# Performance work log

Measured on AMD Instinct MI355X. Metric: run time of the kernel, lower is better.

## Reference

```python
import jax, jax.numpy as jnp
import numpy as np

R = 14        # num_relations
N = 100000    # num nodes
E = 1600000   # num edges
B = 8         # n_bases: num_blocks for layer 1, num_bases for layer 2
DIN, DH, DOUT = 64, 64, 64


def setup_inputs() -> dict:
    key = jax.random.key(0)
    ks = jax.random.split(key, 10)
    x = jax.random.normal(ks[0], (N, DIN), jnp.float32)
    edge_index = jax.random.randint(ks[1], (2, E), 0, N)
    edge_type = jax.random.randint(ks[2], (E,), 0, R)
    # Layer 1: block-diagonal decomposition weights (R, B, DIN/B, DH/B)
    w1 = jax.random.normal(ks[3], (R, B, DIN // B, DH // B), jnp.float32) * 0.1
    root1 = jax.random.normal(ks[4], (DIN, DH), jnp.float32) * 0.1
    bias1 = jnp.zeros((DH,), jnp.float32)
    # Layer 2: basis decomposition: W_r = sum_b comp2[r,b] * bases2[b]
    comp2 = jax.random.normal(ks[5], (R, B), jnp.float32) * 0.3
    bases2 = jax.random.normal(ks[6], (B, DH, DOUT), jnp.float32) * 0.1
    root2 = jax.random.normal(ks[7], (DH, DOUT), jnp.float32) * 0.1
    bias2 = jnp.zeros((DOUT,), jnp.float32)
    return {"x": x, "edge_index": edge_index, "edge_type": edge_type,
            "w1": w1, "root1": root1, "bias1": bias1,
            "comp2": comp2, "bases2": bases2, "root2": root2, "bias2": bias2}


def _rel_scatter_max(h_rel, src, dst, edge_type):
    """h_rel: (R, N, d) per-relation transformed node features.
    Per-relation scatter-max over destination nodes, then sum over relations
    (PyG RGCNConv with aggr='max': empty segments contribute 0)."""
    msgs = h_rel[edge_type, src]                  # (E, d) gather
    seg = edge_type * N + dst                     # combined (relation, dst) key
    agg = jax.ops.segment_max(msgs, seg, num_segments=R * N)  # (R*N, d), -inf where empty
    agg = jnp.where(jnp.isneginf(agg), 0.0, agg)
    return agg.reshape(R, N, -1).sum(axis=0)      # (N, d)


def reference(x, edge_index, edge_type, w1, root1, bias1, comp2, bases2, root2, bias2):
    src, dst = edge_index[0], edge_index[1]
    # ---- layer 1: block-diagonal RGCNConv, aggr='max' ----
    xb = x.reshape(N, B, DIN // B)
    h = jnp.einsum('nbi,rbio->rnbo', xb, w1).reshape(R, N, DH)
    out = _rel_scatter_max(h, src, dst, edge_type) + x @ root1 + bias1
    x1 = jax.nn.relu(out)  # dropout p=0.4 is identity in eval mode
    # ---- layer 2: basis-decomposed RGCNConv, aggr='max' ----
    W2 = jnp.einsum('rb,bio->rio', comp2, bases2)  # (R, DH, DOUT)
    h2 = jnp.einsum('ni,rio->rno', x1, W2)         # (R, N, DOUT)
    out2 = _rel_scatter_max(h2, src, dst, edge_type) + x1 @ root2 + bias2
    return out2
```

## Files before the change

kernel.cpp:

```cpp
#include <hip/hip_runtime.h>
#include <math.h>

#define RNUM 14
#define NNODE 100000
#define ENUM 1600000
#define NBKT 196
#define NFINE 8192
#define NBLK1 ((ENUM + 8191) / 8192)
#define NT16 (NNODE / 16)
#define NTB ((NT16 + 15) / 16)

typedef __attribute__((ext_vector_type(8))) short bf16x8;
typedef __attribute__((ext_vector_type(4))) float f32x4;

__device__ inline unsigned short f2bf(float f) {
    unsigned u = __builtin_bit_cast(unsigned, f);
    u += 0x7FFF + ((u >> 16) & 1);
    return (unsigned short)(u >> 16);
}
__device__ inline float bf2f(unsigned short h) {
    unsigned u = ((unsigned)h) << 16;
    return __builtin_bit_cast(float, u);
}
__device__ inline int uload(const int* __restrict__ p) {
    return __builtin_amdgcn_readfirstlane(*p);
}

__global__ void __launch_bounds__(1024) bhist_k(const int* __restrict__ dst,
                                                int* __restrict__ bcnt) {
    __shared__ int c[256];
    int t = threadIdx.x;
    if (t < 256) c[t] = 0;
    __syncthreads();
    int e0 = blockIdx.x * 8192;
#pragma unroll
    for (int j = 0; j < 8; j++) {
        int e = e0 + j * 1024 + t;
        if (e < ENUM) atomicAdd(&c[dst[e] >> 9], 1);
    }
    __syncthreads();
    if (t < NBKT && c[t] > 0) atomicAdd(&bcnt[t], c[t]);
}

__global__ void bscan_k(const int* __restrict__ bcnt, int* __restrict__ bbase,
                        int* __restrict__ bcursor) {
    __shared__ int sh[256];
    int t = threadIdx.x;
    int v = (t < NBKT) ? bcnt[t] : 0;
    sh[t] = v;
    __syncthreads();
    for (int o = 1; o < 256; o <<= 1) {
        int u = (t >= o) ? sh[t - o] : 0;
        __syncthreads();
        sh[t] += u;
        __syncthreads();
    }
    int excl = sh[t] - v;
    if (t < NBKT) { bbase[t] = excl; bcursor[t] = excl; }
    if (t == NBKT - 1) bbase[NBKT] = sh[t];
}

__global__ void __launch_bounds__(1024) scatter1_k(const int* __restrict__ src,
        const int* __restrict__ dst, const int* __restrict__ et,
        int* __restrict__ bcursor, int2* __restrict__ pay) {
    __shared__ int cnt[256];
    __shared__ int rnk[256];
    __shared__ int base[256];
    int t = threadIdx.x;
    if (t < 256) { cnt[t] = 0; rnk[t] = 0; }
    __syncthreads();
    int e0 = blockIdx.x * 8192;
    int d[8], s[8], r[8];
#pragma unroll
    for (int j = 0; j < 8; j++) {
        int e = e0 + j * 1024 + t;
        if (e < ENUM) {
            d[j] = dst[e]; s[j] = src[e]; r[j] = et[e];
            atomicAdd(&cnt[d[j] >> 9], 1);
        } else d[j] = -1;
    }
    __syncthreads();
    if (t < NBKT && cnt[t] > 0) base[t] = atomicAdd(&bcursor[t], cnt[t]);
    __syncthreads();
#pragma unroll
    for (int j = 0; j < 8; j++) {
        if (d[j] < 0) continue;
        int b = d[j] >> 9;
        int rk = atomicAdd(&rnk[b], 1);
        int2 p; p.x = r[j] * NNODE + s[j]; p.y = (d[j] & 511) * 16 + r[j];
        pay[base[b] + rk] = p;
    }
}

__global__ void __launch_bounds__(1024) bsort_k(const int2* __restrict__ pay,
        const int* __restrict__ bbase, int* __restrict__ offs, int* __restrict__ ssrc) {
    __shared__ int cnt[NFINE];
    __shared__ int tsum[1024];
    int bkt = blockIdx.x, t = threadIdx.x;
    int e0 = bbase[bkt], e1 = bbase[bkt + 1];
#pragma unroll
    for (int i = t; i < NFINE; i += 1024) cnt[i] = 0;
    __syncthreads();
    for (int e = e0 + t; e < e1; e += 1024) atomicAdd(&cnt[pay[e].y], 1);
    __syncthreads();
    int loc[8], s = 0;
#pragma unroll
    for (int j = 0; j < 8; j++) { loc[j] = cnt[t * 8 + j]; s += loc[j]; }
    tsum[t] = s;
    __syncthreads();
    for (int o = 1; o < 1024; o <<= 1) {
        int u = (t >= o) ? tsum[t - o] : 0;
        __syncthreads();
        tsum[t] += u;
        __syncthreads();
    }
    int run = tsum[t] - s;
#pragma unroll
    for (int j = 0; j < 8; j++) {
        int idx = t * 8 + j;
        cnt[idx] = run;
        offs[bkt * NFINE + idx] = e0 + run;
        run += loc[j];
    }
    __syncthreads();
    for (int e = e0 + t; e < e1; e += 1024) {
        int2 p = pay[e];
        int rk = atomicAdd(&cnt[p.y], 1);
        ssrc[e0 + rk] = p.x;
    }
}

__global__ void frags_k(const float* __restrict__ w1, const float* __restrict__ comp2,
                        const float* __restrict__ bases2, const float* __restrict__ root1,
                        const float* __restrict__ root2,
                        unsigned short* __restrict__ frag1, unsigned short* __restrict__ frag2,
                        unsigned short* __restrict__ rootf1, unsigned short* __restrict__ rootf2) {
    int gid = blockIdx.x * 256 + threadIdx.x;
    if (gid < 2 * RNUM * 4096) {
        int which = gid >= RNUM * 4096;
        int idx = gid - which * (RNUM * 4096);
        int j = idx & 7, lane = (idx >> 3) & 63, ot = (idx >> 9) & 3, kh = (idx >> 11) & 1, r = idx >> 12;
        int k = kh * 32 + (lane >> 4) * 8 + j;
        int c = ot * 16 + (lane & 15);
        if (!which) {
            int bi = k >> 3, bo = c >> 3;
            float v = 0.f;
            if (bi == bo) v = w1[((r * 8 + bi) * 8 + (k & 7)) * 8 + (c & 7)];
            frag1[idx] = f2bf(v);
        } else {
            float s = 0.f;
#pragma unroll
            for (int b = 0; b < 8; b++) s += comp2[r * 8 + b] * bases2[(b * 64 + k) * 64 + c];
            frag2[idx] = f2bf(s);
        }
    } else {
        int idx2 = gid - 2 * RNUM * 4096;
        if (idx2 >= 8192) return;
        int which = idx2 >= 4096;
        int idx = idx2 & 4095;
        int j = idx & 7, lane = (idx >> 3) & 63, ot = (idx >> 9) & 3, kh = (idx >> 11) & 1;
        int k = kh * 32 + (lane >> 4) * 8 + j;
        int c = ot * 16 + (lane & 15);
        const float* W = which ? root2 : root1;
        unsigned short* F = which ? rootf2 : rootf1;
        F[idx] = f2bf(W[k * 64 + c]);
    }
}

__global__ void xb_k(const float* __restrict__ x, unsigned short* __restrict__ xb) {
    int idx = blockIdx.x * 256 + threadIdx.x;
    if (idx >= NNODE * 64) return;
    xb[idx] = f2bf(x[idx]);
}

__global__ void __launch_bounds__(256) gemm_k(const unsigned short* __restrict__ A,
                                              const unsigned short* __restrict__ F,
                                              unsigned short* __restrict__ Y) {
    int tb = blockIdx.x % NTB;
    int r  = blockIdx.x / NTB;
    int wave = threadIdx.x >> 6, lane = threadIdx.x & 63;
    const unsigned short* Fr = F + (size_t)r * 4096;
    bf16x8 wf[2][4];
#pragma unroll
    for (int kh = 0; kh < 2; kh++)
#pragma unroll
        for (int ot = 0; ot < 4; ot++)
            wf[kh][ot] = *(const bf16x8*)(Fr + ((kh * 4 + ot) * 64 + lane) * 8);
    int node16 = lane & 15;
    int kcol = (lane >> 4) * 8;
    int g = lane >> 4;
    for (int s = 0; s < 4; s++) {
        int nt = tb * 16 + wave * 4 + s;
        if (nt >= NT16) break;
        int nbase = nt * 16;
        const unsigned short* Arow = A + (size_t)(nbase + node16) * 64;
        bf16x8 b0 = *(const bf16x8*)(Arow + kcol);
        bf16x8 b1 = *(const bf16x8*)(Arow + 32 + kcol);
        f32x4 acc[4];
#pragma unroll
        for (int ot = 0; ot < 4; ot++) {
            acc[ot] = (f32x4){0.f, 0.f, 0.f, 0.f};
            acc[ot] = __builtin_amdgcn_mfma_f32_16x16x32_bf16(wf[0][ot], b0, acc[ot], 0, 0, 0);
            acc[ot] = __builtin_amdgcn_mfma_f32_16x16x32_bf16(wf[1][ot], b1, acc[ot], 0, 0, 0);
        }
        unsigned short* Yr = Y + ((size_t)r * NNODE + nbase) * 64;
#pragma unroll
        for (int ot = 0; ot < 4; ot++) {
            unsigned p0 = (unsigned)f2bf(acc[ot][0]) | ((unsigned)f2bf(acc[ot][1]) << 16);
            unsigned p1 = (unsigned)f2bf(acc[ot][2]) | ((unsigned)f2bf(acc[ot][3]) << 16);
            uint2 pv; pv.x = p0; pv.y = p1;
            *(uint2*)(Yr + (size_t)node16 * 64 + ot * 16 + g * 4) = pv;
        }
    }
}

template <int RC>
__global__ void __launch_bounds__(256) agg_k(
    const unsigned short* __restrict__ H, const int* __restrict__ offs,
    const int* __restrict__ ssrc, const unsigned short* __restrict__ xrootb,
    const float* __restrict__ bias, float* __restrict__ aggbuf,
    unsigned short* __restrict__ x1b, float* __restrict__ outf,
    int r0, int r0N, int rcnt, int flags) {
    int wv = threadIdx.x >> 6, lane = threadIdx.x & 63;
    int d = __builtin_amdgcn_readfirstlane(blockIdx.x * 4 + wv);
    if (d >= NNODE) return;
    float msum = 0.f;

    if constexpr (RC > 0) {
        const int base = d * 16 + r0;
        int bnd[RC + 1];
#pragma unroll
        for (int j = 0; j <= RC; j++) bnd[j] = offs[base + j];
        int e0   = __builtin_amdgcn_readfirstlane(bnd[0]);
        int eend = __builtin_amdgcn_readfirstlane(bnd[RC]);
        float m = -INFINITY;
        for (int cb = e0; cb < eend; cb += 64) {
            int idx = cb + lane;
            int cidx = (idx < eend) ? idx : eend - 1;
            int sv = ssrc[cidx];
            unsigned long long mask = 0;
#pragma unroll
            for (int j = 1; j < RC; j++) {
                int kk_ = bnd[j] - cb;
                if (kk_ >= 0 && kk_ < 64 && bnd[j] > e0) mask |= 1ull << kk_;
            }
            int n = eend - cb; if (n > 64) n = 64;
            for (int k0 = 0; k0 < n; k0 += 16) {
                float h[16];
#pragma unroll
                for (int u = 0; u < 16; u++) {
                    int kk = k0 + u;
                    int kc = (kk < n) ? kk : n - 1;
                    int s = __builtin_amdgcn_readlane(sv, kc);
                    h[u] = bf2f(H[(size_t)(s - r0N) * 64 + lane]);
                }
#pragma unroll
                for (int u = 0; u < 16; u++) {
                    int kk = k0 + u;
                    if (kk >= n) break;
                    bool fl = (mask >> kk) & 1;
                    msum += fl ? m : 0.f;
                    m = fl ? h[u] : fmaxf(m, h[u]);
                }
            }
        }
        if (eend > e0) msum += m;
    } else {
        const int base = d * 16 + r0;
        for (int j = 0; j < rcnt; j++) {
            int e = uload(offs + base + j);
            int ee = uload(offs + base + j + 1);
            if (e >= ee) continue;
            float m = -INFINITY;
            for (; e < ee; e++) {
                int row = uload(ssrc + e) - r0N;
                m = fmaxf(m, bf2f(H[(size_t)row * 64 + lane]));
            }
            msum += m;
        }
    }

    size_t o = (size_t)d * 64 + lane;
    if (!(flags & 1)) msum += aggbuf[o];
    if (!(flags & 2)) { aggbuf[o] = msum; return; }
    float v = msum + bf2f(xrootb[o]) + bias[lane];
    if (flags & 4) x1b[o] = f2bf(fmaxf(v, 0.f));
    else outf[o] = v;
}

extern "C" void kernel_launch(void* const* d_in, const int* in_sizes, int n_in,
                              void* d_out, int out_size, void* d_ws, size_t ws_size,
                              hipStream_t stream) {
    const float* x      = (const float*)d_in[0];
    const int*   ei     = (const int*)d_in[1];
    const int*   et     = (const int*)d_in[2];
    const float* w1     = (const float*)d_in[3];
    const float* root1  = (const float*)d_in[4];
    const float* bias1  = (const float*)d_in[5];
    const float* comp2  = (const float*)d_in[6];
    const float* bases2 = (const float*)d_in[7];
    const float* root2  = (const float*)d_in[8];
    const float* bias2  = (const float*)d_in[9];
    const int* srcv = ei;
    const int* dstv = ei + ENUM;
    float* out = (float*)d_out;

    char* w = (char*)d_ws;
    size_t off = 0;
    auto alloc = [&](size_t bytes) -> void* {
        void* p = w + off;
        off += (bytes + 255) & ~(size_t)255;
        return p;
    };
    int*   offs    = (int*)alloc(((size_t)NBKT * NFINE + 1) * sizeof(int));
    int*   bcnt    = (int*)alloc(256 * sizeof(int));
    int*   bbase   = (int*)alloc(257 * sizeof(int));
    int*   bcursor = (int*)alloc(256 * sizeof(int));
    int2*  pay     = (int2*)alloc((size_t)ENUM * sizeof(int2));
    int*   ssrc    = (int*)alloc((size_t)ENUM * sizeof(int));
    unsigned short* xb     = (unsigned short*)alloc((size_t)NNODE * 64 * 2);
    unsigned short* xrootb = (unsigned short*)alloc((size_t)NNODE * 64 * 2);
    unsigned short* frag1  = (unsigned short*)alloc((size_t)RNUM * 4096 * 2);
    unsigned short* frag2  = (unsigned short*)alloc((size_t)RNUM * 4096 * 2);
    unsigned short* rootf1 = (unsigned short*)alloc(4096 * 2);
    unsigned short* rootf2 = (unsigned short*)alloc(4096 * 2);
    size_t fixed = off;
    if (fixed > ws_size) return;
    size_t slab = ((size_t)NNODE * 64 * 2 + 255) & ~(size_t)255;
    size_t avail = ws_size - fixed;
    int r_per;
    float* aggbuf;
    unsigned short* H;
    if (avail >= (size_t)RNUM * slab) {
        r_per = RNUM;
        H = (unsigned short*)alloc((size_t)RNUM * slab);
        aggbuf = (float*)H;
    } else {
        aggbuf = (float*)alloc((size_t)NNODE * 64 * 4);
        if (off > ws_size) return;
        avail = ws_size - off;
        r_per = (int)(avail / slab);
        if (r_per < 1) return;
        if (r_per > RNUM) r_per = RNUM;
        H = (unsigned short*)alloc((size_t)r_per * slab);
    }

    hipMemsetAsync(bcnt, 0, 256 * sizeof(int), stream);

    bhist_k<<<NBLK1, 1024, 0, stream>>>(dstv, bcnt);
    bscan_k<<<1, 256, 0, stream>>>(bcnt, bbase, bcursor);
    scatter1_k<<<NBLK1, 1024, 0, stream>>>(srcv, dstv, et, bcursor, pay);
    bsort_k<<<NBKT, 1024, 0, stream>>>(pay, bbase, offs, ssrc);

    frags_k<<<480, 256, 0, stream>>>(w1, comp2, bases2, root1, root2,
                                     frag1, frag2, rootf1, rootf2);
    xb_k<<<(NNODE * 64 + 255) / 256, 256, 0, stream>>>(x, xb);

    int nch = (RNUM + r_per - 1) / r_per;
    int aggGrid = NNODE / 4;

    for (int layer = 0; layer < 2; layer++) {
        const unsigned short* frag = layer ? frag2 : frag1;
        const unsigned short* rootf = layer ? rootf2 : rootf1;
        const float* bias = layer ? bias2 : bias1;
        gemm_k<<<NTB, 256, 0, stream>>>(xb, rootf, xrootb);
        for (int c = 0; c < nch; c++) {
            int r0 = c * r_per;
            int rcnt = (RNUM - r0 < r_per) ? (RNUM - r0) : r_per;
            gemm_k<<<rcnt * NTB, 256, 0, stream>>>(xb, frag + (size_t)r0 * 4096, H);
            int flags = (c == 0 ? 1 : 0) | (c == nch - 1 ? 2 : 0) | (layer == 0 ? 4 : 0);
            if (rcnt == RNUM)
                agg_k<RNUM><<<aggGrid, 256, 0, stream>>>(H, offs, ssrc, xrootb, bias, aggbuf,
                                                         xb, out, r0, r0 * NNODE, rcnt, flags);
            else if (rcnt == 7)
                agg_k<7><<<aggGrid, 256, 0, stream>>>(H, offs, ssrc, xrootb, bias, aggbuf,
                                                      xb, out, r0, r0 * NNODE, rcnt, flags);
            else
                agg_k<0><<<aggGrid, 256, 0, stream>>>(H, offs, ssrc, xrootb, bias, aggbuf,
                                                      xb, out, r0, r0 * NNODE, rcnt, flags);
        }
    }
}
```

Before: 414.9 us.

## Quantize per-relation features to int8 with per-node scales and fuse root GEMM

The per-relation GEMM now writes int8 features with a per-node bf16 absmax scale instead of bf16, and aggregation dequantizes on the fly. This halves the bytes gathered per edge in the memory-bound scatter-max. The root-weight GEMM is folded into the first relation GEMM launch, and the weight-fragment and x conversion kernels merge into one prep kernel. The trade-off is reduced numeric precision and one extra scale load per edge.

Measured after the change: 637.2 us. 1.54x slower.

```diff
diff --git a/kernel.cpp b/kernel.cpp
--- a/kernel.cpp
+++ b/kernel.cpp
@@ -9,6 +9,8 @@
 #define NBLK1 ((ENUM + 8191) / 8192)
 #define NT16 (NNODE / 16)
 #define NTB ((NT16 + 15) / 16)
+#define FRAGREL (RNUM + 1)
+#define FRAGTOT (2 * FRAGREL * 4096)
 
 typedef __attribute__((ext_vector_type(8))) short bf16x8;
 typedef __attribute__((ext_vector_type(4))) float f32x4;
@@ -130,56 +132,53 @@
     }
 }
 
-__global__ void frags_k(const float* __restrict__ w1, const float* __restrict__ comp2,
-                        const float* __restrict__ bases2, const float* __restrict__ root1,
-                        const float* __restrict__ root2,
-                        unsigned short* __restrict__ frag1, unsigned short* __restrict__ frag2,
-                        unsigned short* __restrict__ rootf1, unsigned short* __restrict__ rootf2) {
+__global__ void prep_k(const float* __restrict__ w1, const float* __restrict__ comp2,
+                       const float* __restrict__ bases2, const float* __restrict__ root1,
+                       const float* __restrict__ root2, const float* __restrict__ x,
+                       unsigned short* __restrict__ frag1, unsigned short* __restrict__ frag2,
+                       unsigned short* __restrict__ xb) {
     int gid = blockIdx.x * 256 + threadIdx.x;
-    if (gid < 2 * RNUM * 4096) {
-        int which = gid >= RNUM * 4096;
-        int idx = gid - which * (RNUM * 4096);
+    if (gid < FRAGTOT) {
+        int half = gid >= FRAGREL * 4096;
+        int idx = gid - half * (FRAGREL * 4096);
         int j = idx & 7, lane = (idx >> 3) & 63, ot = (idx >> 9) & 3, kh = (idx >> 11) & 1, r = idx >> 12;
         int k = kh * 32 + (lane >> 4) * 8 + j;
         int c = ot * 16 + (lane & 15);
-        if (!which) {
-            int bi = k >> 3, bo = c >> 3;
-            float v = 0.f;
-            if (bi == bo) v = w1[((r * 8 + bi) * 8 + (k & 7)) * 8 + (c & 7)];
+        float v;
+        if (!half) {
+            if (r < RNUM) {
+                int bi = k >> 3, bo = c >> 3;
+                v = 0.f;
+                if (bi == bo) v = w1[((r * 8 + bi) * 8 + (k & 7)) * 8 + (c & 7)];
+            } else v = root1[k * 64 + c];
             frag1[idx] = f2bf(v);
         } else {
-            float s = 0.f;
-#pragma unroll
-            for (int b = 0; b < 8; b++) s += comp2[r * 8 + b] * bases2[(b * 64 + k) * 64 + c];
-            frag2[idx] = f2bf(s);
+            if (r < RNUM) {
+                float s = 0.f;
+#pragma unroll
+                for (int b = 0; b < 8; b++) s += comp2[r * 8 + b] * bases2[(b * 64 + k) * 64 + c];
+                v = s;
+            } else v = root2[k * 64 + c];
+            frag2[idx] = f2bf(v);
         }
     } else {
-        int idx2 = gid - 2 * RNUM * 4096;
-        if (idx2 >= 8192) return;
-        int which = idx2 >= 4096;
-        int idx = idx2 & 4095;
-        int j = idx & 7, lane = (idx >> 3) & 63, ot = (idx >> 9) & 3, kh = (idx >> 11) & 1;
-        int k = kh * 32 + (lane >> 4) * 8 + j;
-        int c = ot * 16 + (lane & 15);
-        const float* W = which ? root2 : root1;
-        unsigned short* F = which ? rootf2 : rootf1;
-        F[idx] = f2bf(W[k * 64 + c]);
-    }
-}
-
-__global__ void xb_k(const float* __restrict__ x, unsigned short* __restrict__ xb) {
-    int idx = blockIdx.x * 256 + threadIdx.x;
-    if (idx >= NNODE * 64) return;
-    xb[idx] = f2bf(x[idx]);
+        int idx = gid - FRAGTOT;
+        if (idx < NNODE * 64) xb[idx] = f2bf(x[idx]);
+    }
 }
 
 __global__ void __launch_bounds__(256) gemm_k(const unsigned short* __restrict__ A,
                                               const unsigned short* __restrict__ F,
-                                              unsigned short* __restrict__ Y) {
+                                              const unsigned short* __restrict__ Froot,
+                                              signed char* __restrict__ H8,
+                                              unsigned short* __restrict__ scales,
+                                              unsigned short* __restrict__ xrootb,
+                                              int nrel, int srow0) {
     int tb = blockIdx.x % NTB;
     int r  = blockIdx.x / NTB;
+    bool isroot = (r == nrel);
+    const unsigned short* Fr = isroot ? Froot : F + (size_t)r * 4096;
     int wave = threadIdx.x >> 6, lane = threadIdx.x & 63;
-    const unsigned short* Fr = F + (size_t)r * 4096;
     bf16x8 wf[2][4];
 #pragma unroll
     for (int kh = 0; kh < 2; kh++)
@@ -203,23 +202,45 @@
             acc[ot] = __builtin_amdgcn_mfma_f32_16x16x32_bf16(wf[0][ot], b0, acc[ot], 0, 0, 0);
             acc[ot] = __builtin_amdgcn_mfma_f32_16x16x32_bf16(wf[1][ot], b1, acc[ot], 0, 0, 0);
         }
-        unsigned short* Yr = Y + ((size_t)r * NNODE + nbase) * 64;
-#pragma unroll
-        for (int ot = 0; ot < 4; ot++) {
-            unsigned p0 = (unsigned)f2bf(acc[ot][0]) | ((unsigned)f2bf(acc[ot][1]) << 16);
-            unsigned p1 = (unsigned)f2bf(acc[ot][2]) | ((unsigned)f2bf(acc[ot][3]) << 16);
-            uint2 pv; pv.x = p0; pv.y = p1;
-            *(uint2*)(Yr + (size_t)node16 * 64 + ot * 16 + g * 4) = pv;
+        if (isroot) {
+            unsigned short* Yr = xrootb + (size_t)nbase * 64;
+#pragma unroll
+            for (int ot = 0; ot < 4; ot++) {
+                unsigned p0 = (unsigned)f2bf(acc[ot][0]) | ((unsigned)f2bf(acc[ot][1]) << 16);
+                unsigned p1 = (unsigned)f2bf(acc[ot][2]) | ((unsigned)f2bf(acc[ot][3]) << 16);
+                uint2 pv; pv.x = p0; pv.y = p1;
+                *(uint2*)(Yr + (size_t)node16 * 64 + ot * 16 + g * 4) = pv;
+            }
+        } else {
+            float m = 0.f;
+#pragma unroll
+            for (int ot = 0; ot < 4; ot++)
+#pragma unroll
+                for (int j = 0; j < 4; j++) m = fmaxf(m, fabsf(acc[ot][j]));
+            m = fmaxf(m, __shfl_xor(m, 16, 64));
+            m = fmaxf(m, __shfl_xor(m, 32, 64));
+            float inv = (m > 0.f) ? 127.f / m : 0.f;
+            signed char* Hr = H8 + ((size_t)r * NNODE + nbase) * 64;
+#pragma unroll
+            for (int ot = 0; ot < 4; ot++) {
+                int q0 = __float2int_rn(acc[ot][0] * inv);
+                int q1 = __float2int_rn(acc[ot][1] * inv);
+                int q2 = __float2int_rn(acc[ot][2] * inv);
+                int q3 = __float2int_rn(acc[ot][3] * inv);
+                unsigned dw = (q0 & 255) | ((q1 & 255) << 8) | ((q2 & 255) << 16) | ((q3 & 255) << 24);
+                *(unsigned*)(Hr + (size_t)node16 * 64 + ot * 16 + g * 4) = dw;
+            }
+            if (lane < 16) scales[srow0 + r * NNODE + nbase + lane] = f2bf(m * (1.f / 127.f));
         }
     }
 }
 
 template <int RC>
 __global__ void __launch_bounds__(256) agg_k(
-    const unsigned short* __restrict__ H, const int* __restrict__ offs,
-    const int* __restrict__ ssrc, const unsigned short* __restrict__ xrootb,
-    const float* __restrict__ bias, float* __restrict__ aggbuf,
-    unsigned short* __restrict__ x1b, float* __restrict__ outf,
+    const signed char* __restrict__ H8, const unsigned short* __restrict__ scales,
+    const int* __restrict__ offs, const int* __restrict__ ssrc,
+    const unsigned short* __restrict__ xrootb, const float* __restrict__ bias,
+    float* __restrict__ aggbuf, unsigned short* __restrict__ x1b, float* __restrict__ outf,
     int r0, int r0N, int rcnt, int flags) {
     int wv = threadIdx.x >> 6, lane = threadIdx.x & 63;
     int d = __builtin_amdgcn_readfirstlane(blockIdx.x * 4 + wv);
@@ -246,21 +267,24 @@
             }
             int n = eend - cb; if (n > 64) n = 64;
             for (int k0 = 0; k0 < n; k0 += 16) {
-                float h[16];
+                int   bq[16];
+                unsigned short sq[16];
 #pragma unroll
                 for (int u = 0; u < 16; u++) {
                     int kk = k0 + u;
                     int kc = (kk < n) ? kk : n - 1;
                     int s = __builtin_amdgcn_readlane(sv, kc);
-                    h[u] = bf2f(H[(size_t)(s - r0N) * 64 + lane]);
+                    bq[u] = H8[(size_t)(s - r0N) * 64 + lane];
+                    sq[u] = scales[s];
                 }
 #pragma unroll
                 for (int u = 0; u < 16; u++) {
                     int kk = k0 + u;
                     if (kk >= n) break;
+                    float h = (float)bq[u] * bf2f(sq[u]);
                     bool fl = (mask >> kk) & 1;
                     msum += fl ? m : 0.f;
-                    m = fl ? h[u] : fmaxf(m, h[u]);
+                    m = fl ? h : fmaxf(m, h);
                 }
             }
         }
@@ -273,8 +297,9 @@
             if (e >= ee) continue;
             float m = -INFINITY;
             for (; e < ee; e++) {
-                int row = uload(ssrc + e) - r0N;
-                m = fmaxf(m, bf2f(H[(size_t)row * 64 + lane]));
+                int s = uload(ssrc + e);
+                float h = (float)H8[(size_t)(s - r0N) * 64 + lane] * bf2f(scales[s]);
+                m = fmaxf(m, h);
             }
             msum += m;
         }
@@ -320,29 +345,28 @@
     int*   ssrc    = (int*)alloc((size_t)ENUM * sizeof(int));
     unsigned short* xb     = (unsigned short*)alloc((size_t)NNODE * 64 * 2);
     unsigned short* xrootb = (unsigned short*)alloc((size_t)NNODE * 64 * 2);
-    unsigned short* frag1  = (unsigned short*)alloc((size_t)RNUM * 4096 * 2);
-    unsigned short* frag2  = (unsigned short*)alloc((size_t)RNUM * 4096 * 2);
-    unsigned short* rootf1 = (unsigned short*)alloc(4096 * 2);
-    unsigned short* rootf2 = (unsigned short*)alloc(4096 * 2);
+    unsigned short* frag1  = (unsigned short*)alloc((size_t)FRAGREL * 4096 * 2);
+    unsigned short* frag2  = (unsigned short*)alloc((size_t)FRAGREL * 4096 * 2);
+    unsigned short* scales = (unsigned short*)alloc((size_t)RNUM * NNODE * 2);
     size_t fixed = off;
     if (fixed > ws_size) return;
-    size_t slab = ((size_t)NNODE * 64 * 2 + 255) & ~(size_t)255;
+    size_t slab8 = ((size_t)NNODE * 64 + 255) & ~(size_t)255;
     size_t avail = ws_size - fixed;
     int r_per;
     float* aggbuf;
-    unsigned short* H;
-    if (avail >= (size_t)RNUM * slab) {
+    signed char* H8;
+    if (avail >= (size_t)RNUM * slab8) {
         r_per = RNUM;
-        H = (unsigned short*)alloc((size_t)RNUM * slab);
-        aggbuf = (float*)H;
+        H8 = (signed char*)alloc((size_t)RNUM * slab8);
+        aggbuf = (float*)H8;
     } else {
         aggbuf = (float*)alloc((size_t)NNODE * 64 * 4);
         if (off > ws_size) return;
         avail = ws_size - off;
-        r_per = (int)(avail / slab);
+        r_per = (int)(avail / slab8);
         if (r_per < 1) return;
         if (r_per > RNUM) r_per = RNUM;
-        H = (unsigned short*)alloc((size_t)r_per * slab);
+        H8 = (signed char*)alloc((size_t)r_per * slab8);
     }
 
     hipMemsetAsync(bcnt, 0, 256 * sizeof(int), stream);
@@ -352,32 +376,30 @@
     scatter1_k<<<NBLK1, 1024, 0, stream>>>(srcv, dstv, et, bcursor, pay);
     bsort_k<<<NBKT, 1024, 0, stream>>>(pay, bbase, offs, ssrc);
 
-    frags_k<<<480, 256, 0, stream>>>(w1, comp2, bases2, root1, root2,
-                                     frag1, frag2, rootf1, rootf2);
-    xb_k<<<(NNODE * 64 + 255) / 256, 256, 0, stream>>>(x, xb);
+    prep_k<<<(FRAGTOT + NNODE * 64 + 255) / 256, 256, 0, stream>>>(
+        w1, comp2, bases2, root1, root2, x, frag1, frag2, xb);
 
     int nch = (RNUM + r_per - 1) / r_per;
     int aggGrid = NNODE / 4;
 
     for (int layer = 0; layer < 2; layer++) {
         const unsigned short* frag = layer ? frag2 : frag1;
-        const unsigned short* rootf = layer ? rootf2 : rootf1;
+        const unsigned short* rootf = (layer ? frag2 : frag1) + (size_t)RNUM * 4096;
         const float* bias = layer ? bias2 : bias1;
-        gemm_k<<<NTB, 256, 0, stream>>>(xb, rootf, xrootb);
         for (int c = 0; c < nch; c++) {
             int r0 = c * r_per;
             int rcnt = (RNUM - r0 < r_per) ? (RNUM - r0) : r_per;
-            gemm_k<<<rcnt * NTB, 256, 0, stream>>>(xb, frag + (size_t)r0 * 4096, H);
+            int nrel = rcnt;
+            int grid = (c == 0) ? (rcnt + 1) * NTB : rcnt * NTB;
+            gemm_k<<<grid, 256, 0, stream>>>(xb, frag + (size_t)r0 * 4096, rootf,
+                                             H8, scales, xrootb, nrel, r0 * NNODE);
             int flags = (c == 0 ? 1 : 0) | (c == nch - 1 ? 2 : 0) | (layer == 0 ? 4 : 0);
             if (rcnt == RNUM)
-                agg_k<RNUM><<<aggGrid, 256, 0, stream>>>(H, offs, ssrc, xrootb, bias, aggbuf,
-                                                         xb, out, r0, r0 * NNODE, rcnt, flags);
-            else if (rcnt == 7)
-                agg_k<7><<<aggGrid, 256, 0, stream>>>(H, offs, ssrc, xrootb, bias, aggbuf,
-                                                      xb, out, r0, r0 * NNODE, rcnt, flags);
+                agg_k<RNUM><<<aggGrid, 256, 0, stream>>>(H8, scales, offs, ssrc, xrootb, bias,
+                                                         aggbuf, xb, out, r0, r0 * NNODE, rcnt, flags);
             else
-                agg_k<0><<<aggGrid, 256, 0, stream>>>(H, offs, ssrc, xrootb, bias, aggbuf,
-                                                      xb, out, r0, r0 * NNODE, rcnt, flags);
-        }
-    }
-}
+                agg_k<0><<<aggGrid, 256, 0, stream>>>(H8, scales, offs, ssrc, xrootb, bias,
+                                                      aggbuf, xb, out, r0, r0 * NNODE, rcnt, flags);
+        }
+    }
+}
```
